# Kernel tuning notes

Hardware: AMD Instinct MI355X
Metric: run time of the kernel (lower is better)

Reference implementation:

```python
import jax, jax.numpy as jnp
import numpy as np

B, T, C, H = 2, 2048, 1024, 16
D = C // H  # head dim = 64


def setup_inputs() -> dict:
    key = jax.random.key(0)
    k1, k2, k3 = jax.random.split(key, 3)
    x = jax.random.normal(k1, (B, T, C), dtype=jnp.float32)
    w_attn = jax.random.normal(k2, (C, 3 * C), dtype=jnp.float32) * (1.0 / np.sqrt(C))
    b_attn = jnp.zeros((3 * C,), dtype=jnp.float32)
    w_proj = jax.random.normal(k3, (C, C), dtype=jnp.float32) * (1.0 / np.sqrt(C))
    b_proj = jnp.zeros((C,), dtype=jnp.float32)
    return {"x": x, "w_attn": w_attn, "b_attn": b_attn, "w_proj": w_proj, "b_proj": b_proj}


def reference(x, w_attn, b_attn, w_proj, b_proj):
    Bx, Tx, Cx = x.shape
    qkv = x @ w_attn + b_attn  # [B, T, 3C]
    q, k, v = jnp.split(qkv, 3, axis=-1)
    # [B, H, T, D]
    q = q.reshape(Bx, Tx, H, D).swapaxes(1, 2)
    k = k.reshape(Bx, Tx, H, D).swapaxes(1, 2)
    v = v.reshape(Bx, Tx, H, D).swapaxes(1, 2)
    scale = 1.0 / jnp.sqrt(jnp.float32(D))
    att = jnp.einsum('bhqd,bhkd->bhqk', q, k) * scale  # [B, H, T, T]
    causal = jnp.tril(jnp.ones((Tx, Tx), dtype=bool))
    att = jnp.where(causal[None, None], att, -jnp.inf)
    att = jax.nn.softmax(att, axis=-1)
    y = jnp.einsum('bhqk,bhkd->bhqd', att, v)  # [B, H, T, D]
    y = y.swapaxes(1, 2).reshape(Bx, Tx, Cx)
    return y @ w_proj + b_proj
```

## Files before the change

### kernel.cpp

```cpp
#include <hip/hip_runtime.h>
#include <hip/hip_bf16.h>


typedef __attribute__((ext_vector_type(8))) short short8x;
typedef __attribute__((ext_vector_type(4))) float float4x;
typedef __attribute__((ext_vector_type(4))) unsigned short ushort4x;
typedef __attribute__((ext_vector_type(2))) unsigned int uint2x;

#define MFMA_BF16 __builtin_amdgcn_mfma_f32_16x16x32_bf16

typedef const __attribute__((address_space(1))) void gvoid_t;
typedef __attribute__((address_space(3))) void lvoid_t;
#define GLOAD_LDS16(g, l) __builtin_amdgcn_global_load_lds((gvoid_t*)(g), (lvoid_t*)(l), 16, 0, 0)

__device__ __forceinline__ unsigned short f2b(float f) {
    unsigned int u = __float_as_uint(f);
    u = (u + 0x7FFFu + ((u >> 16) & 1u)) >> 16;
    return (unsigned short)u;
}
__device__ __forceinline__ unsigned int pk2(float a, float b) {
    return __builtin_amdgcn_perm(__float_as_uint(b) + 0x8000u,
                                 __float_as_uint(a) + 0x8000u, 0x07060302u);
}

__device__ __forceinline__ void stage32(const unsigned short* g, size_t rs,
                                        short* ldst, int w0, int lane) {
    const int r8 = lane >> 3;
    const int sc = ((lane & 7) ^ r8) * 8;
#pragma unroll
    for (int q = 0; q < 4; q++) {
        GLOAD_LDS16(g + (size_t)(w0 + q * 8 + r8) * rs + sc,
                    ldst + (w0 + q * 8) * 64);
    }
}

__global__ __launch_bounds__(256) void prep(const float* __restrict__ x,
                                            unsigned short* __restrict__ xb,
                                            const float* __restrict__ wa,
                                            unsigned short* __restrict__ waT,
                                            const float* __restrict__ wp,
                                            unsigned short* __restrict__ wpT) {
    __shared__ float tile[32][33];
    const int blk = blockIdx.x;
    if (blk < 4096) {
        int i = blk * 256 + threadIdx.x;
        float4 v = ((const float4*)x)[i];
        ushort4x o = { f2b(v.x), f2b(v.y), f2b(v.z), f2b(v.w) };
        ((ushort4x*)xb)[i] = o;
        return;
    }
    int idx = blk - 4096;
    int bx = idx & 127;
    int by = idx >> 7;
    const float* in;
    unsigned short* outp;
    int cols;
    if (bx < 96) { in = wa; outp = waT; cols = 3072; }
    else         { in = wp; outp = wpT; cols = 1024; bx -= 96; }
    const int tx = threadIdx.x & 31, ty = threadIdx.x >> 5;
    const int cbase = bx * 32, rbase = by * 32;
    int c = cbase + tx;
    for (int j = 0; j < 32; j += 8)
        tile[ty + j][tx] = in[(size_t)(rbase + ty + j) * cols + c];
    __syncthreads();
    int rr = rbase + tx;
    for (int j = 0; j < 32; j += 8) {
        int cc = cbase + ty + j;
        outp[(size_t)cc * 1024 + rr] = f2b(tile[tx][ty + j]);
    }
}

template <bool SWAP>
__device__ __forceinline__ void qkv_mainloop(const unsigned short* Ag,
                                             const unsigned short* Bg,
                                             short* lA, short* lB,
                                             float4x (&acc)[4][4],
                                             int wave, int lane, int wr, int wc,
                                             int quad, int l16, int sw) {
    const int K = 1024;
    for (int kk = 0; kk < K; kk += 64) {
        stage32(Ag + kk, K, lA, wave * 32, lane);
        stage32(Bg + kk, K, lB, wave * 32, lane);
        __syncthreads();

#pragma unroll
        for (int kk2 = 0; kk2 < 2; kk2++) {
            short8x a[4], b[4];
#pragma unroll
            for (int i = 0; i < 4; i++)
                a[i] = *(const short8x*)&lA[(wr * 64 + i * 16 + l16) * 64 +
                                            ((kk2 * 4 + quad) ^ sw) * 8];
#pragma unroll
            for (int j = 0; j < 4; j++)
                b[j] = *(const short8x*)&lB[(wc * 64 + j * 16 + l16) * 64 +
                                            ((kk2 * 4 + quad) ^ sw) * 8];
#pragma unroll
            for (int i = 0; i < 4; i++)
#pragma unroll
                for (int j = 0; j < 4; j++)
                    acc[i][j] = SWAP ? MFMA_BF16(b[j], a[i], acc[i][j], 0, 0, 0)
                                     : MFMA_BF16(a[i], b[j], acc[i][j], 0, 0, 0);
        }
        __syncthreads();
    }
}

__global__ __launch_bounds__(256, 4) void gemm_qkv(const unsigned short* __restrict__ A,
                                                   const unsigned short* __restrict__ BT,
                                                   const float* __restrict__ bias,
                                                   unsigned short* __restrict__ QK,
                                                   unsigned short* __restrict__ VTg) {
    __shared__ union {
        struct { short A[128 * 64]; short B[128 * 64]; } s;
        short vt[4][64 * 80];
    } lds;

    const int K = 1024;
    const int lane = threadIdx.x & 63;
    const int wave = threadIdx.x >> 6;
    const int quad = lane >> 4;
    const int l16  = lane & 15;
    const int sw   = l16 & 7;

    const int rblk = blockIdx.y * 128;
    const int cblk = blockIdx.x * 128;
    const int wr = wave >> 1, wc = wave & 1;
    const bool qk = (blockIdx.x < 16);

    float4x acc[4][4] = {};

    const unsigned short* Ag = A  + (size_t)rblk * K;
    const unsigned short* Bg = BT + (size_t)cblk * K;

    if (qk) qkv_mainloop<true >(Ag, Bg, lds.s.A, lds.s.B, acc, wave, lane, wr, wc, quad, l16, sw);
    else    qkv_mainloop<false>(Ag, Bg, lds.s.A, lds.s.B, acc, wave, lane, wr, wc, quad, l16, sw);

    const int rbase = rblk + wr * 64;
    const int cbase = cblk + wc * 64;

    if (qk) {
        const float sc = (blockIdx.x < 8) ? 0.18033688f : 1.0f;
#pragma unroll
        for (int i = 0; i < 4; i++) {
            const int r = rbase + i * 16 + l16;
#pragma unroll
            for (int j = 0; j < 4; j++) {
                const int c = cbase + j * 16 + quad * 4;
                float4 bv = *(const float4*)&bias[c];
                uint2x p = { pk2((acc[i][j][0] + bv.x) * sc, (acc[i][j][1] + bv.y) * sc),
                             pk2((acc[i][j][2] + bv.z) * sc, (acc[i][j][3] + bv.w) * sc) };
                *(uint2x*)&QK[(size_t)r * 2048 + c] = p;
            }
        }
    } else {
#pragma unroll
        for (int i = 0; i < 4; i++) {
#pragma unroll
            for (int j = 0; j < 4; j++) {
                int c = cbase + j * 16 + l16;
                float bv = bias[c];
                uint2x p = { pk2(acc[i][j][0] + bv, acc[i][j][1] + bv),
                             pk2(acc[i][j][2] + bv, acc[i][j][3] + bv) };
                *(uint2x*)&lds.vt[wave][(j * 16 + l16) * 80 + i * 16 + quad * 4] = p;
            }
        }
        const int h   = (cbase - 2048) >> 6;
        const int hb  = (rbase >> 11) * 16 + h;
        const int tb0 = rbase & 2047;
#pragma unroll
        for (int p = 0; p < 8; p++) {
            int dd   = p * 8 + (lane >> 3);
            int toff = (lane & 7) * 8;
            short8x vv = *(const short8x*)&lds.vt[wave][dd * 80 + toff];
            *(short8x*)&VTg[((size_t)(hb * 64 + dd)) * 2048 + tb0 + toff] = vv;
        }
    }
}

__global__ __launch_bounds__(256) void gemm_proj(const unsigned short* __restrict__ A,
                                                 const unsigned short* __restrict__ BT,
                                                 const float* __restrict__ bias,
                                                 float* __restrict__ out) {
    __shared__ struct { short A[64 * 64]; short B[128 * 64]; } lds;

    const int K = 1024, N = 1024;
    const int lane = threadIdx.x & 63;
    const int wave = threadIdx.x >> 6;
    const int quad = lane >> 4;
    const int l16  = lane & 15;
    const int sw   = l16 & 7;

    const int rblk = blockIdx.y * 64;
    const int cblk = blockIdx.x * 128;

    float4x acc[4][2] = {};

    const unsigned short* Ag = A  + (size_t)rblk * K;
    const unsigned short* Bg = BT + (size_t)cblk * K;

    for (int kk = 0; kk < K; kk += 64) {
        if (wave < 2) {
            stage32(Ag + kk, K, lds.A, wave * 32, lane);
        } else {
            stage32(Bg + kk, K, lds.B, (wave - 2) * 64, lane);
            stage32(Bg + kk, K, lds.B, (wave - 2) * 64 + 32, lane);
        }
        __syncthreads();

#pragma unroll
        for (int kk2 = 0; kk2 < 2; kk2++) {
            short8x b[2];
#pragma unroll
            for (int j = 0; j < 2; j++)
                b[j] = *(const short8x*)&lds.B[(wave * 32 + j * 16 + l16) * 64 +
                                               ((kk2 * 4 + quad) ^ sw) * 8];
#pragma unroll
            for (int i = 0; i < 4; i++) {
                short8x a = *(const short8x*)&lds.A[(i * 16 + l16) * 64 +
                                                    ((kk2 * 4 + quad) ^ sw) * 8];
#pragma unroll
                for (int j = 0; j < 2; j++)
                    acc[i][j] = MFMA_BF16(a, b[j], acc[i][j], 0, 0, 0);
            }
        }
        __syncthreads();
    }

#pragma unroll
    for (int j = 0; j < 2; j++) {
        const int c = cblk + wave * 32 + j * 16 + l16;
        const float bv = bias[c];
#pragma unroll
        for (int i = 0; i < 4; i++) {
#pragma unroll
            for (int reg = 0; reg < 4; reg++) {
                int r = rblk + i * 16 + quad * 4 + reg;
                out[(size_t)r * N + c] = acc[i][j][reg] + bv;
            }
        }
    }
}

__global__ __launch_bounds__(256) void attn_kernel(const unsigned short* __restrict__ QK,
                                                   const unsigned short* __restrict__ VT,
                                                   unsigned short* __restrict__ Y) {
    __shared__ __attribute__((aligned(16))) short Kl[2][64 * 64];
    __shared__ __attribute__((aligned(16))) short Vl[2][64 * 64];
    __shared__ __attribute__((aligned(16))) short Pl[4][16 * 64];

    const int tid  = threadIdx.x;
    const int lane = tid & 63;
    const int wave = tid >> 6;
    const int quad = lane >> 4;
    const int l16  = lane & 15;
    const int sw   = l16 & 7;

    const int bid = blockIdx.x;
    const int v2  = (bid >> 8) & 3;
    const int s2  = ((bid >> 3) & 3) ^ v2;
    const int m3  = (bid >> 5) & 7;
    const int qb  = (s2 == 0) ? m3 : (s2 == 1) ? 15 - m3
                  : (s2 == 2) ? 16 + m3 : 31 - m3;
    const int bh  = (bid & 7) | (v2 << 3);
    const int b = bh >> 4, h = bh & 15;

    const unsigned short* Qp = QK + ((size_t)b * 2048) * 2048 + h * 64;
    const unsigned short* Kp = Qp + 1024;
    const unsigned short* Vp = VT + (size_t)bh * 64 * 2048;

    const int qbase = qb * 64 + wave * 16;
    const int ntb   = qb + 1;

    short8x aq[2];
#pragma unroll
    for (int kk = 0; kk < 2; kk++)
        aq[kk] = *(const short8x*)(Qp + (size_t)(qbase + l16) * 2048 + kk * 32 + quad * 8);

    const short ONE = (short)0x3F80;
    const short8x ones = { ONE, ONE, ONE, ONE, ONE, ONE, ONE, ONE };

    if (wave < 2) stage32(Kp, 2048, Kl[0], wave * 32, lane);
    else          stage32(Vp, 2048, Vl[0], (wave - 2) * 32, lane);
    __syncthreads();

    float4x lacc = {};
    float4x O[4] = {};

    for (int it = 0; it < ntb; it++) {
        const int kb = it * 64;
        const short* Kc = Kl[it & 1];
        const short* Vc = Vl[it & 1];

        if (it + 1 < ntb) {
            const int kb2 = kb + 64;
            if (wave < 2) stage32(Kp + (size_t)kb2 * 2048, 2048, Kl[(it + 1) & 1], wave * 32, lane);
            else          stage32(Vp + kb2, 2048, Vl[(it + 1) & 1], (wave - 2) * 32, lane);
        }

        float4x S[4];
#pragma unroll
        for (int t = 0; t < 4; t++) {
            short8x kf0 = *(const short8x*)&Kc[(t * 16 + l16) * 64 + ((quad) ^ sw) * 8];
            short8x kf1 = *(const short8x*)&Kc[(t * 16 + l16) * 64 + ((4 + quad) ^ sw) * 8];
            S[t] = (float4x){0.f, 0.f, 0.f, 0.f};
            S[t] = MFMA_BF16(kf0, aq[0], S[t], 0, 0, 0);
            S[t] = MFMA_BF16(kf1, aq[1], S[t], 0, 0, 0);
        }

        if (kb + 64 > qbase) {
            int q = qbase + l16;
#pragma unroll
            for (int t = 0; t < 4; t++)
#pragma unroll
                for (int reg = 0; reg < 4; reg++)
                    if (kb + t * 16 + quad * 4 + reg > q) S[t][reg] = -1e38f;
        }

#pragma unroll
        for (int t = 0; t < 4; t++) {
            float e0 = __builtin_amdgcn_exp2f(S[t][0]);
            float e1 = __builtin_amdgcn_exp2f(S[t][1]);
            float e2 = __builtin_amdgcn_exp2f(S[t][2]);
            float e3 = __builtin_amdgcn_exp2f(S[t][3]);
            uint2x p = { pk2(e0, e1), pk2(e2, e3) };
            *(uint2x*)&Pl[wave][l16 * 64 + ((2 * t + (quad >> 1)) ^ sw) * 8 + (quad & 1) * 4] = p;
        }

#pragma unroll
        for (int kc = 0; kc < 2; kc++) {
            short8x bp = *(const short8x*)&Pl[wave][l16 * 64 + ((4 * kc + quad) ^ sw) * 8];
            lacc = MFMA_BF16(ones, bp, lacc, 0, 0, 0);
#pragma unroll
            for (int dt = 0; dt < 4; dt++) {
                short8x vf = *(const short8x*)&Vc[(dt * 16 + l16) * 64 + ((kc * 4 + quad) ^ sw) * 8];
                O[dt] = MFMA_BF16(vf, bp, O[dt], 0, 0, 0);
            }
        }
        __syncthreads();
    }

    float rl = 1.0f / lacc[0];
#pragma unroll
    for (int dt = 0; dt < 4; dt++) {
        uint2x o = { pk2(O[dt][0] * rl, O[dt][1] * rl),
                     pk2(O[dt][2] * rl, O[dt][3] * rl) };
        *(uint2x*)&Pl[wave][l16 * 64 + ((2 * dt + (quad >> 1)) ^ sw) * 8 + (quad & 1) * 4] = o;
    }
    const int t = qbase + l16;
#pragma unroll
    for (int cc = 0; cc < 2; cc++) {
        short8x row = *(const short8x*)&Pl[wave][l16 * 64 + ((2 * quad + cc) ^ sw) * 8];
        *(short8x*)&Y[((size_t)(b * 2048 + t)) * 1024 + h * 64 + (2 * quad + cc) * 8] = row;
    }
}

extern "C" void kernel_launch(void* const* d_in, const int* in_sizes, int n_in,
                              void* d_out, int out_size, void* d_ws, size_t ws_size,
                              hipStream_t stream) {
    const float* x      = (const float*)d_in[0];
    const float* w_attn = (const float*)d_in[1];
    const float* b_attn = (const float*)d_in[2];
    const float* w_proj = (const float*)d_in[3];
    const float* b_proj = (const float*)d_in[4];
    float* out = (float*)d_out;

    char* ws = (char*)d_ws;
    unsigned short* xb  = (unsigned short*)(ws + (size_t)0);
    unsigned short* waT = (unsigned short*)(ws + (size_t)(8  << 20));
    unsigned short* wpT = (unsigned short*)(ws + (size_t)(14 << 20));
    unsigned short* QKb = (unsigned short*)(ws + (size_t)(16 << 20));
    unsigned short* VTb = (unsigned short*)(ws + (size_t)(32 << 20));
    unsigned short* yb  = (unsigned short*)(ws + (size_t)(40 << 20));

    prep<<<8192, 256, 0, stream>>>(x, xb, w_attn, waT, w_proj, wpT);

    gemm_qkv<<<dim3(24, 32), 256, 0, stream>>>(xb, waT, b_attn, QKb, VTb);

    attn_kernel<<<1024, 256, 0, stream>>>(QKb, VTb, yb);

    gemm_proj<<<dim3(8, 64), 256, 0, stream>>>(yb, wpT, b_proj, out);
}
```

Before: 171.3 us.

## Double-buffer QKV GEMM LDS stages with K=32 tiles and prefetch

```diff
diff --git a/kernel.cpp b/kernel.cpp
--- a/kernel.cpp
+++ b/kernel.cpp
@@ -31,6 +31,17 @@
     for (int q = 0; q < 4; q++) {
         GLOAD_LDS16(g + (size_t)(w0 + q * 8 + r8) * rs + sc,
                     ldst + (w0 + q * 8) * 64);
+    }
+}
+
+__device__ __forceinline__ void stage32k32(const unsigned short* g, size_t rs,
+                                           short* ldst, int w0, int lane) {
+    const int r4 = lane >> 2;
+    const int sc = ((lane & 3) ^ ((lane >> 3) & 3)) * 8;
+#pragma unroll
+    for (int q = 0; q < 2; q++) {
+        GLOAD_LDS16(g + (size_t)(w0 + q * 16 + r4) * rs + sc,
+                    ldst + (w0 + q * 16) * 32);
     }
 }
 
@@ -76,31 +87,34 @@
                                              short* lA, short* lB,
                                              float4x (&acc)[4][4],
                                              int wave, int lane, int wr, int wc,
-                                             int quad, int l16, int sw) {
+                                             int quad, int l16) {
     const int K = 1024;
-    for (int kk = 0; kk < K; kk += 64) {
-        stage32(Ag + kk, K, lA, wave * 32, lane);
-        stage32(Bg + kk, K, lB, wave * 32, lane);
-        __syncthreads();
-
-#pragma unroll
-        for (int kk2 = 0; kk2 < 2; kk2++) {
-            short8x a[4], b[4];
-#pragma unroll
-            for (int i = 0; i < 4; i++)
-                a[i] = *(const short8x*)&lA[(wr * 64 + i * 16 + l16) * 64 +
-                                            ((kk2 * 4 + quad) ^ sw) * 8];
+    const int co = (quad ^ ((l16 >> 1) & 3)) * 8;
+
+    stage32k32(Ag, K, lA, wave * 32, lane);
+    stage32k32(Bg, K, lB, wave * 32, lane);
+    __syncthreads();
+
+    for (int it = 0; it < 32; ++it) {
+        const short* As = lA + (it & 1) * (128 * 32);
+        const short* Bs = lB + (it & 1) * (128 * 32);
+        if (it + 1 < 32) {
+            stage32k32(Ag + (it + 1) * 32, K, lA + ((it + 1) & 1) * (128 * 32), wave * 32, lane);
+            stage32k32(Bg + (it + 1) * 32, K, lB + ((it + 1) & 1) * (128 * 32), wave * 32, lane);
+        }
+        short8x a[4], b[4];
+#pragma unroll
+        for (int i = 0; i < 4; i++)
+            a[i] = *(const short8x*)&As[(wr * 64 + i * 16 + l16) * 32 + co];
+#pragma unroll
+        for (int j = 0; j < 4; j++)
+            b[j] = *(const short8x*)&Bs[(wc * 64 + j * 16 + l16) * 32 + co];
+#pragma unroll
+        for (int i = 0; i < 4; i++)
 #pragma unroll
             for (int j = 0; j < 4; j++)
-                b[j] = *(const short8x*)&lB[(wc * 64 + j * 16 + l16) * 64 +
-                                            ((kk2 * 4 + quad) ^ sw) * 8];
-#pragma unroll
-            for (int i = 0; i < 4; i++)
-#pragma unroll
-                for (int j = 0; j < 4; j++)
-                    acc[i][j] = SWAP ? MFMA_BF16(b[j], a[i], acc[i][j], 0, 0, 0)
-                                     : MFMA_BF16(a[i], b[j], acc[i][j], 0, 0, 0);
-        }
+                acc[i][j] = SWAP ? MFMA_BF16(b[j], a[i], acc[i][j], 0, 0, 0)
+                                 : MFMA_BF16(a[i], b[j], acc[i][j], 0, 0, 0);
         __syncthreads();
     }
 }
@@ -111,7 +125,7 @@
                                                    unsigned short* __restrict__ QK,
                                                    unsigned short* __restrict__ VTg) {
     __shared__ union {
-        struct { short A[128 * 64]; short B[128 * 64]; } s;
+        struct { short A[2][128 * 32]; short B[2][128 * 32]; } s;
         short vt[4][64 * 80];
     } lds;
 
@@ -120,7 +134,6 @@
     const int wave = threadIdx.x >> 6;
     const int quad = lane >> 4;
     const int l16  = lane & 15;
-    const int sw   = l16 & 7;
 
     const int rblk = blockIdx.y * 128;
     const int cblk = blockIdx.x * 128;
@@ -132,8 +145,8 @@
     const unsigned short* Ag = A  + (size_t)rblk * K;
     const unsigned short* Bg = BT + (size_t)cblk * K;
 
-    if (qk) qkv_mainloop<true >(Ag, Bg, lds.s.A, lds.s.B, acc, wave, lane, wr, wc, quad, l16, sw);
-    else    qkv_mainloop<false>(Ag, Bg, lds.s.A, lds.s.B, acc, wave, lane, wr, wc, quad, l16, sw);
+    if (qk) qkv_mainloop<true >(Ag, Bg, lds.s.A[0], lds.s.B[0], acc, wave, lane, wr, wc, quad, l16);
+    else    qkv_mainloop<false>(Ag, Bg, lds.s.A[0], lds.s.B[0], acc, wave, lane, wr, wc, quad, l16);
 
     const int rbase = rblk + wr * 64;
     const int cbase = cblk + wc * 64;
```

After: 172.9 us. Within noise of the previous version (+1.0%).

## Double attention query tile per block to 128 rows, reusing K/V tiles across two query subtiles

Applied to the files above, without the earlier changes.

```diff
diff --git a/kernel.cpp b/kernel.cpp
--- a/kernel.cpp
+++ b/kernel.cpp
@@ -241,12 +241,12 @@
     }
 }
 
-__global__ __launch_bounds__(256) void attn_kernel(const unsigned short* __restrict__ QK,
-                                                   const unsigned short* __restrict__ VT,
-                                                   unsigned short* __restrict__ Y) {
+__global__ __launch_bounds__(256, 3) void attn_kernel(const unsigned short* __restrict__ QK,
+                                                      const unsigned short* __restrict__ VT,
+                                                      unsigned short* __restrict__ Y) {
     __shared__ __attribute__((aligned(16))) short Kl[2][64 * 64];
     __shared__ __attribute__((aligned(16))) short Vl[2][64 * 64];
-    __shared__ __attribute__((aligned(16))) short Pl[4][16 * 64];
+    __shared__ __attribute__((aligned(16))) short Pl[4][2][16 * 64];
 
     const int tid  = threadIdx.x;
     const int lane = tid & 63;
@@ -256,25 +256,27 @@
     const int sw   = l16 & 7;
 
     const int bid = blockIdx.x;
-    const int v2  = (bid >> 8) & 3;
-    const int s2  = ((bid >> 3) & 3) ^ v2;
-    const int m3  = (bid >> 5) & 7;
-    const int qb  = (s2 == 0) ? m3 : (s2 == 1) ? 15 - m3
-                  : (s2 == 2) ? 16 + m3 : 31 - m3;
-    const int bh  = (bid & 7) | (v2 << 3);
+    const int v1  = (bid >> 8) & 1;
+    const int s1  = ((bid >> 3) & 1) ^ v1;
+    const int m3  = (bid >> 4) & 7;
+    const int qb  = s1 ? 15 - m3 : m3;
+    const int bh  = (bid & 7) | (((bid >> 7) & 1) << 3) | (v1 << 4);
     const int b = bh >> 4, h = bh & 15;
 
     const unsigned short* Qp = QK + ((size_t)b * 2048) * 2048 + h * 64;
     const unsigned short* Kp = Qp + 1024;
     const unsigned short* Vp = VT + (size_t)bh * 64 * 2048;
 
-    const int qbase = qb * 64 + wave * 16;
-    const int ntb   = qb + 1;
-
-    short8x aq[2];
-#pragma unroll
-    for (int kk = 0; kk < 2; kk++)
-        aq[kk] = *(const short8x*)(Qp + (size_t)(qbase + l16) * 2048 + kk * 32 + quad * 8);
+    const int qw  = qb * 128 + wave * 32;
+    const int ntb = 2 * qb + 2;
+
+    short8x aq[2][2];
+#pragma unroll
+    for (int qt = 0; qt < 2; qt++)
+#pragma unroll
+        for (int kk = 0; kk < 2; kk++)
+            aq[qt][kk] = *(const short8x*)(Qp + (size_t)(qw + qt * 16 + l16) * 2048 +
+                                           kk * 32 + quad * 8);
 
     const short ONE = (short)0x3F80;
     const short8x ones = { ONE, ONE, ONE, ONE, ONE, ONE, ONE, ONE };
@@ -283,8 +285,8 @@
     else          stage32(Vp, 2048, Vl[0], (wave - 2) * 32, lane);
     __syncthreads();
 
-    float4x lacc = {};
-    float4x O[4] = {};
+    float4x lacc[2] = {};
+    float4x O[4][2] = {};
 
     for (int it = 0; it < ntb; it++) {
         const int kb = it * 64;
@@ -297,60 +299,70 @@
             else          stage32(Vp + kb2, 2048, Vl[(it + 1) & 1], (wave - 2) * 32, lane);
         }
 
-        float4x S[4];
-#pragma unroll
-        for (int t = 0; t < 4; t++) {
-            short8x kf0 = *(const short8x*)&Kc[(t * 16 + l16) * 64 + ((quad) ^ sw) * 8];
-            short8x kf1 = *(const short8x*)&Kc[(t * 16 + l16) * 64 + ((4 + quad) ^ sw) * 8];
-            S[t] = (float4x){0.f, 0.f, 0.f, 0.f};
-            S[t] = MFMA_BF16(kf0, aq[0], S[t], 0, 0, 0);
-            S[t] = MFMA_BF16(kf1, aq[1], S[t], 0, 0, 0);
-        }
-
-        if (kb + 64 > qbase) {
-            int q = qbase + l16;
-#pragma unroll
-            for (int t = 0; t < 4; t++)
-#pragma unroll
-                for (int reg = 0; reg < 4; reg++)
-                    if (kb + t * 16 + quad * 4 + reg > q) S[t][reg] = -1e38f;
-        }
-
-#pragma unroll
-        for (int t = 0; t < 4; t++) {
-            float e0 = __builtin_amdgcn_exp2f(S[t][0]);
-            float e1 = __builtin_amdgcn_exp2f(S[t][1]);
-            float e2 = __builtin_amdgcn_exp2f(S[t][2]);
-            float e3 = __builtin_amdgcn_exp2f(S[t][3]);
-            uint2x p = { pk2(e0, e1), pk2(e2, e3) };
-            *(uint2x*)&Pl[wave][l16 * 64 + ((2 * t + (quad >> 1)) ^ sw) * 8 + (quad & 1) * 4] = p;
-        }
-
-#pragma unroll
-        for (int kc = 0; kc < 2; kc++) {
-            short8x bp = *(const short8x*)&Pl[wave][l16 * 64 + ((4 * kc + quad) ^ sw) * 8];
-            lacc = MFMA_BF16(ones, bp, lacc, 0, 0, 0);
-#pragma unroll
-            for (int dt = 0; dt < 4; dt++) {
-                short8x vf = *(const short8x*)&Vc[(dt * 16 + l16) * 64 + ((kc * 4 + quad) ^ sw) * 8];
-                O[dt] = MFMA_BF16(vf, bp, O[dt], 0, 0, 0);
-            }
-        }
-        __syncthreads();
-    }
-
-    float rl = 1.0f / lacc[0];
-#pragma unroll
-    for (int dt = 0; dt < 4; dt++) {
-        uint2x o = { pk2(O[dt][0] * rl, O[dt][1] * rl),
-                     pk2(O[dt][2] * rl, O[dt][3] * rl) };
-        *(uint2x*)&Pl[wave][l16 * 64 + ((2 * dt + (quad >> 1)) ^ sw) * 8 + (quad & 1) * 4] = o;
-    }
-    const int t = qbase + l16;
-#pragma unroll
-    for (int cc = 0; cc < 2; cc++) {
-        short8x row = *(const short8x*)&Pl[wave][l16 * 64 + ((2 * quad + cc) ^ sw) * 8];
-        *(short8x*)&Y[((size_t)(b * 2048 + t)) * 1024 + h * 64 + (2 * quad + cc) * 8] = row;
+        if (kb <= qw + 31) {
+#pragma unroll
+            for (int qt = 0; qt < 2; qt++) {
+                const int qbase = qw + qt * 16;
+#pragma unroll
+                for (int t = 0; t < 4; t++) {
+                    short8x kf0 = *(const short8x*)&Kc[(t * 16 + l16) * 64 + ((quad) ^ sw) * 8];
+                    short8x kf1 = *(const short8x*)&Kc[(t * 16 + l16) * 64 + ((4 + quad) ^ sw) * 8];
+                    float4x S = (float4x){0.f, 0.f, 0.f, 0.f};
+                    S = MFMA_BF16(kf0, aq[qt][0], S, 0, 0, 0);
+                    S = MFMA_BF16(kf1, aq[qt][1], S, 0, 0, 0);
+
+                    if (kb + 64 > qbase) {
+                        int q = qbase + l16;
+#pragma unroll
+                        for (int reg = 0; reg < 4; reg++)
+                            if (kb + t * 16 + quad * 4 + reg > q) S[reg] = -1e38f;
+                    }
+
+                    float e0 = __builtin_amdgcn_exp2f(S[0]);
+                    float e1 = __builtin_amdgcn_exp2f(S[1]);
+                    float e2 = __builtin_amdgcn_exp2f(S[2]);
+                    float e3 = __builtin_amdgcn_exp2f(S[3]);
+                    uint2x p = { pk2(e0, e1), pk2(e2, e3) };
+                    *(uint2x*)&Pl[wave][qt][l16 * 64 + ((2 * t + (quad >> 1)) ^ sw) * 8 +
+                                            (quad & 1) * 4] = p;
+                }
+            }
+
+#pragma unroll
+            for (int kc = 0; kc < 2; kc++) {
+                short8x vf[4];
+#pragma unroll
+                for (int dt = 0; dt < 4; dt++)
+                    vf[dt] = *(const short8x*)&Vc[(dt * 16 + l16) * 64 + ((kc * 4 + quad) ^ sw) * 8];
+#pragma unroll
+                for (int qt = 0; qt < 2; qt++) {
+                    short8x bp = *(const short8x*)&Pl[wave][qt][l16 * 64 + ((4 * kc + quad) ^ sw) * 8];
+                    lacc[qt] = MFMA_BF16(ones, bp, lacc[qt], 0, 0, 0);
+#pragma unroll
+                    for (int dt = 0; dt < 4; dt++)
+                        O[dt][qt] = MFMA_BF16(vf[dt], bp, O[dt][qt], 0, 0, 0);
+                }
+            }
+        }
+        __syncthreads();
+    }
+
+#pragma unroll
+    for (int qt = 0; qt < 2; qt++) {
+        float rl = 1.0f / lacc[qt][0];
+#pragma unroll
+        for (int dt = 0; dt < 4; dt++) {
+            uint2x o = { pk2(O[dt][qt][0] * rl, O[dt][qt][1] * rl),
+                         pk2(O[dt][qt][2] * rl, O[dt][qt][3] * rl) };
+            *(uint2x*)&Pl[wave][qt][l16 * 64 + ((2 * dt + (quad >> 1)) ^ sw) * 8 +
+                                    (quad & 1) * 4] = o;
+        }
+        const int t = qw + qt * 16 + l16;
+#pragma unroll
+        for (int cc = 0; cc < 2; cc++) {
+            short8x row = *(const short8x*)&Pl[wave][qt][l16 * 64 + ((2 * quad + cc) ^ sw) * 8];
+            *(short8x*)&Y[((size_t)(b * 2048 + t)) * 1024 + h * 64 + (2 * quad + cc) * 8] = row;
+        }
     }
 }
 
@@ -376,7 +388,7 @@
 
     gemm_qkv<<<dim3(24, 32), 256, 0, stream>>>(xb, waT, b_attn, QKb, VTb);
 
-    attn_kernel<<<1024, 256, 0, stream>>>(QKb, VTb, yb);
+    attn_kernel<<<512, 256, 0, stream>>>(QKb, VTb, yb);
 
     gemm_proj<<<dim3(8, 64), 256, 0, stream>>>(yb, wpT, b_proj, out);
 }
```

Result: slower. 174.8 us (+2.1%).
